# Kernel tuning notes

Hardware: AMD Instinct MI355X
Metric: run time of the kernel (lower is better)

Reference implementation:

```python
import jax, jax.numpy as jnp
import numpy as np

EPSILON = 0.001
PROXIMITY_THRESHOLD = 0.15


def setup_inputs() -> dict:
    key = jax.random.key(0)
    k1, k2, k3 = jax.random.split(key, 3)
    B, N, E = 8, 512, 4096
    node_positions = jax.random.uniform(k1, (B, N, 2), dtype=jnp.float32)
    adjacency = jax.random.normal(k2, (B, N, N), dtype=jnp.float32)
    edge_index = jax.random.randint(k3, (2, E), 0, B * N, dtype=jnp.int64)
    return {"node_positions": node_positions, "adjacency": adjacency, "edge_index": edge_index}


def _candidate_mask(pos, src, dst, batch, prox):
    # pos: (BN,2); src/dst/batch: (E,)
    p_src = pos[src]
    p_dst = pos[dst]
    mid = (p_src + p_dst) * 0.5                      # (E,2)
    half = jnp.linalg.norm(p_dst - p_src, axis=-1) * 0.5  # (E,)
    dist = jnp.linalg.norm(mid[:, None] - mid[None, :], axis=-1)  # (E,E)
    reach = half[:, None] + half[None, :] + prox
    E = src.shape[0]
    idx = jnp.arange(E)
    upper = idx[None, :] > idx[:, None]              # ei < ej
    same_batch = batch[:, None] == batch[None, :]
    shares = ((src[:, None] == src[None, :]) | (src[:, None] == dst[None, :])
              | (dst[:, None] == src[None, :]) | (dst[:, None] == dst[None, :]))
    return (dist < reach) & upper & same_batch & ~shares


def _segment_distance_dense(p_src, p_dst):
    # All-pairs closest-approach distance between segments i and j.
    d1 = p_dst - p_src                               # (E,2)
    sq = jnp.maximum((d1 * d1).sum(-1), 1e-12)       # (E,)
    a = sq[:, None]                                  # a_i
    e = sq[None, :]                                  # e_j
    b = d1 @ d1.T                                    # (E,E) d1_i . d1_j
    d1_dot_a1 = (d1 * p_src).sum(-1)                 # (E,) d1_k . a1_k
    c = d1_dot_a1[:, None] - d1 @ p_src.T            # d1_i . (a1_i - b1_j)
    f = p_src @ d1.T - d1_dot_a1[None, :]            # d1_j . (a1_i - b1_j)
    denom = jnp.maximum(a * e - b * b, 1e-12)
    s = (b * f - c * e) / denom
    t = (a * f - b * c) / denom
    s = jnp.clip(s, 0.0, 1.0)
    t = jnp.clip(t, 0.0, 1.0)
    t = jnp.clip((b * s + f) / e, 0.0, 1.0)
    s = jnp.clip((b * t - c) / a, 0.0, 1.0)
    closest_a = p_src[:, None, :] + s[..., None] * d1[:, None, :]   # (E,E,2)
    closest_b = p_src[None, :, :] + t[..., None] * d1[None, :, :]   # (E,E,2)
    return jnp.linalg.norm(closest_a - closest_b, axis=-1)          # (E,E)


def reference(node_positions, adjacency, edge_index):
    # adjacency is accepted (per the torch forward signature) but unused by this axiom.
    B, N, _ = node_positions.shape
    pos = node_positions.reshape(-1, 2)              # (B*N, 2)
    src = edge_index[0]
    dst = edge_index[1]
    batch = src // N                                 # (E,) batch membership per edge
    mask = jax.lax.stop_gradient(
        _candidate_mask(jax.lax.stop_gradient(pos), src, dst, batch, PROXIMITY_THRESHOLD))
    dmin = _segment_distance_dense(pos[src], pos[dst])  # (E,E)
    pair_loss = jax.nn.relu(EPSILON - dmin) * mask.astype(dmin.dtype)
    n_pairs = mask.sum()
    loss = pair_loss.sum() / jnp.maximum(n_pairs, 1).astype(dmin.dtype)
    violation_mask = mask & (pair_loss > 0)
    violation_scores = jax.lax.stop_gradient(pair_loss)
    return loss, violation_mask, violation_scores
```

## Files before the change

kernel.cpp:

```cpp
#include <hip/hip_runtime.h>


#define EDGES   4096
#define LOGE    12
#define EPS     0.001f
#define PROX    0.15f
#define NBUCKET 2048
#define ACHUNK  16
#define MAXC    1024

__global__ __launch_bounds__(256) void edge_pre(
    const float2* __restrict__ pos,
    const int*    __restrict__ esrc,
    const int*    __restrict__ edst,
    float4* __restrict__ rec1, float4* __restrict__ rec2, float4* __restrict__ rec3,
    unsigned* __restrict__ bcount)
{
#pragma clang fp contract(off)
    const int e = blockIdx.x * 256 + threadIdx.x;
    const int s = esrc[e], d = edst[e];
    const float2 a1 = pos[s], a2 = pos[d];
    const float d1x = a2.x - a1.x, d1y = a2.y - a1.y;
    const float midx = (a1.x + a2.x) * 0.5f, midy = (a1.y + a2.y) * 0.5f;
    const float half = sqrtf(d1x * d1x + d1y * d1y) * 0.5f;
    const float sq   = fmaxf(d1x * d1x + d1y * d1y, 1e-12f);
    const float dda  = d1x * a1.x + d1y * a1.y;
    rec1[e] = make_float4(a1.x, a1.y, d1x, d1y);
    rec2[e] = make_float4(midx, midy, half, dda);
    rec3[e] = make_float4(sq, __int_as_float(s), __int_as_float(d), 0.0f);

    const int bv   = s >> 9;
    const int lane = threadIdx.x & 63;
    #pragma unroll
    for (int v = 0; v < 8; ++v) {
        const unsigned long long mk = __ballot(bv == v);
        if (mk && lane == (__ffsll((long long)mk) - 1))
            atomicAdd(&bcount[v], (unsigned)__popcll(mk));
    }
}

#define ZF_BLOCKS 2048
#define ZF_T      (ZF_BLOCKS * 256)
#define ZF_QUADS  8388607u
__global__ __launch_bounds__(256) void zero_fill(
    float* __restrict__ out,
    const unsigned* __restrict__ bcount, unsigned* __restrict__ boffset)
{
    const unsigned g = blockIdx.x * 256 + threadIdx.x;
    if (g == 0) {
        unsigned acc = 0;
        #pragma unroll
        for (int v = 0; v < 8; ++v) { boffset[v] = acc; acc += bcount[v]; }
        out[1] = 0.0f; out[2] = 0.0f; out[3] = 0.0f;
        out[2 * EDGES * EDGES] = 0.0f;
    }
    float4* __restrict__ base = (float4*)(out + 4);
    const float4 z4 = make_float4(0.0f, 0.0f, 0.0f, 0.0f);
    #pragma unroll
    for (unsigned p = 0; p < 16; ++p) {
        const unsigned idx = g + p * (unsigned)ZF_T;
        if (idx < ZF_QUADS) base[idx] = z4;
    }
}

__global__ __launch_bounds__(256) void edge_scatter(
    const float4* __restrict__ rec1, const float4* __restrict__ rec2,
    const float4* __restrict__ rec3,
    const unsigned* __restrict__ boffset, unsigned* __restrict__ bcursor,
    float4* __restrict__ srec1, float4* __restrict__ srec2,
    float4* __restrict__ srec3, unsigned* __restrict__ sorig)
{
    const int e    = blockIdx.x * 256 + threadIdx.x;
    const int lane = threadIdx.x & 63;
    const unsigned long long ltmask = (1ull << lane) - 1ull;
    const float4 r3 = rec3[e];
    const int bv = __float_as_int(r3.y) >> 9;

    unsigned slot = 0;
    #pragma unroll
    for (int v = 0; v < 8; ++v) {
        const unsigned long long mk = __ballot(bv == v);
        if (mk) {
            const int leader = __ffsll((long long)mk) - 1;
            unsigned basev = 0;
            if (lane == leader) basev = atomicAdd(&bcursor[v], (unsigned)__popcll(mk));
            basev = (unsigned)__shfl((int)basev, leader, 64);
            if (bv == v) slot = boffset[v] + basev + (unsigned)__popcll(mk & ltmask);
        }
    }
    srec1[slot] = rec1[e];
    srec2[slot] = rec2[e];
    srec3[slot] = r3;
    sorig[slot] = (unsigned)e;
}

__global__ __launch_bounds__(256) void pair_kernel(
    const float4* __restrict__ srec1, const float4* __restrict__ srec2,
    const float4* __restrict__ srec3, const unsigned* __restrict__ sorig,
    const unsigned* __restrict__ bcount, const unsigned* __restrict__ boffset,
    float* __restrict__ out,
    float* __restrict__ bsum, unsigned* __restrict__ bcnt)
{
#pragma clang fp contract(off)
    const int bz   = blockIdx.z;
    const int cnt  = (int)bcount[bz];
    const int off  = (int)boffset[bz];
    const int abase = blockIdx.x * ACHUNK;
    const int bbase = blockIdx.y * 256;
    if (abase >= cnt || bbase >= cnt) return;
    if (abase >= bbase + 256) return;

    float* __restrict__ o_mask  = out + 1;
    float* __restrict__ o_score = out + 1 + EDGES * EDGES;

    const int tid  = threadIdx.x;
    const int bidx = bbase + tid;
    const bool havb = bidx < cnt;

    float4 br1, br2, br3; int ob = 0;
    if (havb) {
        br1 = srec1[off + bidx]; br2 = srec2[off + bidx]; br3 = srec3[off + bidx];
        ob  = (int)sorig[off + bidx];
    }
    const int bs = havb ? __float_as_int(br3.y) : -1;
    const int bd = havb ? __float_as_int(br3.z) : -1;

    float vsum = 0.0f;
    int   vcnt = 0;

    const int aend = (abase + ACHUNK < cnt) ? abase + ACHUNK : cnt;
    for (int aa = abase; aa < aend; ++aa) {
        const int slotA = off + aa;
        const float4 ar1 = srec1[slotA], ar2 = srec2[slotA], ar3 = srec3[slotA];
        const int oa = (int)sorig[slotA];
        const int as_ = __float_as_int(ar3.y), ad = __float_as_int(ar3.z);

        const bool act = havb && (aa < bidx);
        if (!__ballot(act)) continue;
        if (act) {
            const float dmx = ar2.x - br2.x, dmy = ar2.y - br2.y;
            const float dist  = sqrtf(dmx * dmx + dmy * dmy);
            const float reach = ar2.z + br2.z + PROX;
            const bool shares = (as_ == bs) | (as_ == bd) | (ad == bs) | (ad == bd);
            const bool m = (dist < reach) & (!shares);
            vcnt += m ? 1 : 0;
            if (m) {
                const bool ai = oa < ob;
                const float4 r1i = ai ? ar1 : br1, r2i = ai ? ar2 : br2, r3i = ai ? ar3 : br3;
                const float4 r1j = ai ? br1 : ar1, r2j = ai ? br2 : ar2, r3j = ai ? br3 : ar3;

                const float sqi = r3i.x, sqj = r3j.x;
                const float b = r1i.z * r1j.z + r1i.w * r1j.w;
                const float c = r2i.w - (r1i.z * r1j.x + r1i.w * r1j.y);
                const float f = (r1i.x * r1j.z + r1i.y * r1j.w) - r2j.w;
                const float denom = fmaxf(sqi * sqj - b * b, 1e-12f);

                float s = (b * f - c * sqj) / denom;
                s = fminf(fmaxf(s, 0.0f), 1.0f);
                const float t = fminf(fmaxf((b * s + f) / sqj, 0.0f), 1.0f);
                s = fminf(fmaxf((b * t - c) / sqi, 0.0f), 1.0f);

                const float cax = r1i.x + s * r1i.z, cay = r1i.y + s * r1i.w;
                const float cbx = r1j.x + t * r1j.z, cby = r1j.y + t * r1j.w;
                const float dx = cax - cbx, dy = cay - cby;
                const float dmin = sqrtf(dx * dx + dy * dy);

                const float pl = fmaxf(EPS - dmin, 0.0f);
                if (pl > 0.0f) {
                    const int io = ai ? oa : ob, jo = ai ? ob : oa;
                    const int k  = (io << LOGE) | jo;
                    o_mask[k]  = 1.0f;
                    o_score[k] = pl;
                    vsum += pl;
                }
            }
        }
    }

    #pragma unroll
    for (int o = 32; o > 0; o >>= 1) {
        vsum += __shfl_xor(vsum, o, 64);
        vcnt += __shfl_xor(vcnt, o, 64);
    }
    __shared__ float    ls[4];
    __shared__ unsigned lc[4];
    const int wid = tid >> 6, lane = tid & 63;
    if (lane == 0) { ls[wid] = vsum; lc[wid] = (unsigned)vcnt; }
    __syncthreads();
    if (tid == 0) {
        const float    s4 = ls[0] + ls[1] + ls[2] + ls[3];
        const unsigned c4 = lc[0] + lc[1] + lc[2] + lc[3];
        if (s4 != 0.0f || c4 != 0u) {
            const int bk = (((blockIdx.z * gridDim.y + blockIdx.y) * gridDim.x) + blockIdx.x) & (NBUCKET - 1);
            atomicAdd(&bsum[bk], s4);
            atomicAdd(&bcnt[bk], c4);
        }
    }
}

__global__ __launch_bounds__(256) void finalize_kernel(
    const float* __restrict__ bsum, const unsigned* __restrict__ bcnt,
    float* __restrict__ out)
{
    float    s = 0.0f;
    unsigned c = 0u;
    for (int b = threadIdx.x; b < NBUCKET; b += 256) { s += bsum[b]; c += bcnt[b]; }
    #pragma unroll
    for (int o = 32; o > 0; o >>= 1) {
        s += __shfl_xor(s, o, 64);
        c += (unsigned)__shfl_xor((int)c, o, 64);
    }
    __shared__ float    ls[4];
    __shared__ unsigned lc[4];
    const int wid = threadIdx.x >> 6, lane = threadIdx.x & 63;
    if (lane == 0) { ls[wid] = s; lc[wid] = c; }
    __syncthreads();
    if (threadIdx.x == 0) {
        const float    st = ls[0] + ls[1] + ls[2] + ls[3];
        const unsigned ct = lc[0] + lc[1] + lc[2] + lc[3];
        const unsigned n  = ct > 1u ? ct : 1u;
        out[0] = st / (float)n;
    }
}

extern "C" void kernel_launch(void* const* d_in, const int* in_sizes, int n_in,
                              void* d_out, int out_size, void* d_ws, size_t ws_size,
                              hipStream_t stream) {
    const float2* pos  = (const float2*)d_in[0];
    const int*    esrc = (const int*)d_in[2];
    const int*    edst = esrc + EDGES;

    float*    out     = (float*)d_out;
    char*     ws      = (char*)d_ws;
    float*    bsum    = (float*)ws;
    unsigned* bcnt    = (unsigned*)(ws + 8192);
    unsigned* bcount  = (unsigned*)(ws + 16384);
    unsigned* boffset = (unsigned*)(ws + 16384 + 32);
    unsigned* bcursor = (unsigned*)(ws + 16384 + 64);
    float4*   rec1    = (float4*)(ws + 32768);
    float4*   rec2    = rec1 + EDGES;
    float4*   rec3    = rec2 + EDGES;
    float4*   srec1   = rec3 + EDGES;
    float4*   srec2   = srec1 + EDGES;
    float4*   srec3   = srec2 + EDGES;
    unsigned* sorig   = (unsigned*)(srec3 + EDGES);

    hipMemsetAsync(d_ws, 0, 16384 + 96, stream);

    edge_pre<<<EDGES / 256, 256, 0, stream>>>(pos, esrc, edst, rec1, rec2, rec3, bcount);
    zero_fill<<<ZF_BLOCKS, 256, 0, stream>>>(out, bcount, boffset);
    edge_scatter<<<EDGES / 256, 256, 0, stream>>>(rec1, rec2, rec3, boffset, bcursor,
                                                  srec1, srec2, srec3, sorig);
    dim3 grid(MAXC / ACHUNK, MAXC / 256, 8);
    pair_kernel<<<grid, 256, 0, stream>>>(srec1, srec2, srec3, sorig,
                                          bcount, boffset, out, bsum, bcnt);
    finalize_kernel<<<1, 256, 0, stream>>>(bsum, bcnt, out);
}
```

Before: 206.7 us.

## Assign one block per B edge and stride threads over earlier A edges

The pair kernel's work decomposition is restructured. Each block now owns one sorted edge b within a batch, and its threads stride over all edges a < b, replacing the old tiles of 16 A edges by 256 B edges that looped serially over A with ballot skipping. rec1 and the original index are now loaded only for candidate pairs that pass the mask test, which cuts global loads. The trade-off is many blocks with very little work when b is small, and heavy load imbalance across blocks, since block b does b comparisons.

Result: faster. 183.1 us (-11.4%).

```diff
diff --git a/kernel.cpp b/kernel.cpp
--- a/kernel.cpp
+++ b/kernel.cpp
@@ -6,7 +6,6 @@
 #define EPS     0.001f
 #define PROX    0.15f
 #define NBUCKET 2048
-#define ACHUNK  16
 #define MAXC    1024
 
 __global__ __launch_bounds__(256) void edge_pre(
@@ -102,77 +101,64 @@
     float* __restrict__ bsum, unsigned* __restrict__ bcnt)
 {
 #pragma clang fp contract(off)
-    const int bz   = blockIdx.z;
-    const int cnt  = (int)bcount[bz];
-    const int off  = (int)boffset[bz];
-    const int abase = blockIdx.x * ACHUNK;
-    const int bbase = blockIdx.y * 256;
-    if (abase >= cnt || bbase >= cnt) return;
-    if (abase >= bbase + 256) return;
+    const int bz  = blockIdx.y;
+    const int b   = blockIdx.x;
+    const int cnt = (int)bcount[bz];
+    if (b == 0 || b >= cnt) return;
+    const int off = (int)boffset[bz];
 
     float* __restrict__ o_mask  = out + 1;
     float* __restrict__ o_score = out + 1 + EDGES * EDGES;
 
-    const int tid  = threadIdx.x;
-    const int bidx = bbase + tid;
-    const bool havb = bidx < cnt;
-
-    float4 br1, br2, br3; int ob = 0;
-    if (havb) {
-        br1 = srec1[off + bidx]; br2 = srec2[off + bidx]; br3 = srec3[off + bidx];
-        ob  = (int)sorig[off + bidx];
-    }
-    const int bs = havb ? __float_as_int(br3.y) : -1;
-    const int bd = havb ? __float_as_int(br3.z) : -1;
+    const float4 br1 = srec1[off + b], br2 = srec2[off + b], br3 = srec3[off + b];
+    const int ob = (int)sorig[off + b];
+    const int bs = __float_as_int(br3.y), bd = __float_as_int(br3.z);
 
     float vsum = 0.0f;
     int   vcnt = 0;
 
-    const int aend = (abase + ACHUNK < cnt) ? abase + ACHUNK : cnt;
-    for (int aa = abase; aa < aend; ++aa) {
-        const int slotA = off + aa;
-        const float4 ar1 = srec1[slotA], ar2 = srec2[slotA], ar3 = srec3[slotA];
-        const int oa = (int)sorig[slotA];
+    for (int a = threadIdx.x; a < b; a += 256) {
+        const int slotA = off + a;
+        const float4 ar2 = srec2[slotA];
+        const float4 ar3 = srec3[slotA];
         const int as_ = __float_as_int(ar3.y), ad = __float_as_int(ar3.z);
 
-        const bool act = havb && (aa < bidx);
-        if (!__ballot(act)) continue;
-        if (act) {
-            const float dmx = ar2.x - br2.x, dmy = ar2.y - br2.y;
-            const float dist  = sqrtf(dmx * dmx + dmy * dmy);
-            const float reach = ar2.z + br2.z + PROX;
-            const bool shares = (as_ == bs) | (as_ == bd) | (ad == bs) | (ad == bd);
-            const bool m = (dist < reach) & (!shares);
-            vcnt += m ? 1 : 0;
-            if (m) {
-                const bool ai = oa < ob;
-                const float4 r1i = ai ? ar1 : br1, r2i = ai ? ar2 : br2, r3i = ai ? ar3 : br3;
-                const float4 r1j = ai ? br1 : ar1, r2j = ai ? br2 : ar2, r3j = ai ? br3 : ar3;
-
-                const float sqi = r3i.x, sqj = r3j.x;
-                const float b = r1i.z * r1j.z + r1i.w * r1j.w;
-                const float c = r2i.w - (r1i.z * r1j.x + r1i.w * r1j.y);
-                const float f = (r1i.x * r1j.z + r1i.y * r1j.w) - r2j.w;
-                const float denom = fmaxf(sqi * sqj - b * b, 1e-12f);
-
-                float s = (b * f - c * sqj) / denom;
-                s = fminf(fmaxf(s, 0.0f), 1.0f);
-                const float t = fminf(fmaxf((b * s + f) / sqj, 0.0f), 1.0f);
-                s = fminf(fmaxf((b * t - c) / sqi, 0.0f), 1.0f);
-
-                const float cax = r1i.x + s * r1i.z, cay = r1i.y + s * r1i.w;
-                const float cbx = r1j.x + t * r1j.z, cby = r1j.y + t * r1j.w;
-                const float dx = cax - cbx, dy = cay - cby;
-                const float dmin = sqrtf(dx * dx + dy * dy);
-
-                const float pl = fmaxf(EPS - dmin, 0.0f);
-                if (pl > 0.0f) {
-                    const int io = ai ? oa : ob, jo = ai ? ob : oa;
-                    const int k  = (io << LOGE) | jo;
-                    o_mask[k]  = 1.0f;
-                    o_score[k] = pl;
-                    vsum += pl;
-                }
+        const float dmx = ar2.x - br2.x, dmy = ar2.y - br2.y;
+        const float dist  = sqrtf(dmx * dmx + dmy * dmy);
+        const float reach = ar2.z + br2.z + PROX;
+        const bool shares = (as_ == bs) | (as_ == bd) | (ad == bs) | (ad == bd);
+        const bool m = (dist < reach) & (!shares);
+        vcnt += m ? 1 : 0;
+        if (m) {
+            const float4 ar1 = srec1[slotA];
+            const int oa = (int)sorig[slotA];
+            const bool ai = oa < ob;
+            const float4 r1i = ai ? ar1 : br1, r2i = ai ? ar2 : br2, r3i = ai ? ar3 : br3;
+            const float4 r1j = ai ? br1 : ar1, r2j = ai ? br2 : ar2, r3j = ai ? br3 : ar3;
+
+            const float sqi = r3i.x, sqj = r3j.x;
+            const float bb = r1i.z * r1j.z + r1i.w * r1j.w;
+            const float c  = r2i.w - (r1i.z * r1j.x + r1i.w * r1j.y);
+            const float f  = (r1i.x * r1j.z + r1i.y * r1j.w) - r2j.w;
+            const float denom = fmaxf(sqi * sqj - bb * bb, 1e-12f);
+
+            float s = (bb * f - c * sqj) / denom;
+            s = fminf(fmaxf(s, 0.0f), 1.0f);
+            const float t = fminf(fmaxf((bb * s + f) / sqj, 0.0f), 1.0f);
+            s = fminf(fmaxf((bb * t - c) / sqi, 0.0f), 1.0f);
+
+            const float cax = r1i.x + s * r1i.z, cay = r1i.y + s * r1i.w;
+            const float cbx = r1j.x + t * r1j.z, cby = r1j.y + t * r1j.w;
+            const float dx = cax - cbx, dy = cay - cby;
+            const float dmin = sqrtf(dx * dx + dy * dy);
+
+            const float pl = fmaxf(EPS - dmin, 0.0f);
+            if (pl > 0.0f) {
+                const int io = ai ? oa : ob, jo = ai ? ob : oa;
+                const int k  = (io << LOGE) | jo;
+                o_mask[k]  = 1.0f;
+                o_score[k] = pl;
+                vsum += pl;
             }
         }
     }
@@ -184,14 +170,14 @@
     }
     __shared__ float    ls[4];
     __shared__ unsigned lc[4];
-    const int wid = tid >> 6, lane = tid & 63;
+    const int wid = threadIdx.x >> 6, lane = threadIdx.x & 63;
     if (lane == 0) { ls[wid] = vsum; lc[wid] = (unsigned)vcnt; }
     __syncthreads();
-    if (tid == 0) {
+    if (threadIdx.x == 0) {
         const float    s4 = ls[0] + ls[1] + ls[2] + ls[3];
         const unsigned c4 = lc[0] + lc[1] + lc[2] + lc[3];
         if (s4 != 0.0f || c4 != 0u) {
-            const int bk = (((blockIdx.z * gridDim.y + blockIdx.y) * gridDim.x) + blockIdx.x) & (NBUCKET - 1);
+            const int bk = (blockIdx.y * MAXC + blockIdx.x) & (NBUCKET - 1);
             atomicAdd(&bsum[bk], s4);
             atomicAdd(&bcnt[bk], c4);
         }
@@ -251,7 +237,7 @@
     zero_fill<<<ZF_BLOCKS, 256, 0, stream>>>(out, bcount, boffset);
     edge_scatter<<<EDGES / 256, 256, 0, stream>>>(rec1, rec2, rec3, boffset, bcursor,
                                                   srec1, srec2, srec3, sorig);
-    dim3 grid(MAXC / ACHUNK, MAXC / 256, 8);
+    dim3 grid(MAXC, 8);
     pair_kernel<<<grid, 256, 0, stream>>>(srec1, srec2, srec3, sorig,
                                           bcount, boffset, out, bsum, bcnt);
     finalize_kernel<<<1, 256, 0, stream>>>(bsum, bcnt, out);
```
